# Performance work log

Hardware: AMD Instinct MI355X
Metric: run time of the kernel (lower is better)

Reference implementation:

```python
import jax, jax.numpy as jnp
import numpy as np

RCUT, RCUT_SMTH = 6.0, 0.5
SEL = [32, 64]
SEC = [0, 32, 96]
PAIRS = [(0, 0), (0, 1), (1, 1)]  # (ti, tj) with ti <= tj, matching stacked weight index
NF, NLOC, NALL = 1, 256, 512
NNEI = sum(SEL)
NG = 96


def setup_inputs() -> dict:
    key = jax.random.key(0)
    ks = jax.random.split(key, 10)
    # coords in a 4A cube so most neighbor distances are inside rcut=6
    extended_coord = jax.random.uniform(ks[0], (NF, NALL * 3), dtype=jnp.float32) * 4.0
    nl = jax.random.randint(ks[1], (NF, NLOC, NNEI), 0, NALL - 1)
    # shift indices >= own local index by 1 to avoid self-neighbors (zero distance)
    nlist = nl + (nl >= jnp.arange(NLOC)[None, :, None]).astype(nl.dtype)
    extended_atype = jax.random.randint(ks[2], (NF, NALL), 0, 2)
    mean = jnp.zeros((2, NNEI, 4), jnp.float32)
    stddev = jnp.ones((2, NNEI, 4), jnp.float32)
    def w(k, shape, fan):
        return jax.random.normal(k, shape, jnp.float32) / np.float32(np.sqrt(fan))
    W1 = w(ks[3], (3, 1, 24), 1.0)
    b1 = 0.1 * jax.random.normal(ks[4], (3, 24), jnp.float32)
    W2 = w(ks[5], (3, 24, 48), 24.0)
    b2 = 0.1 * jax.random.normal(ks[6], (3, 48), jnp.float32)
    W3 = w(ks[7], (3, 48, 96), 48.0)
    b3 = 0.1 * jax.random.normal(ks[8], (3, 96), jnp.float32)
    return dict(nlist=nlist, extended_coord=extended_coord, extended_atype=extended_atype,
                mean=mean, stddev=stddev, W1=W1, b1=b1, W2=W2, b2=b2, W3=W3, b3=b3)


def _smooth_weight(r, rmin, rmax):
    uu = (r - rmin) / (rmax - rmin)
    vv = uu * uu * uu * (-6.0 * uu * uu + 15.0 * uu - 10.0) + 1.0
    return jnp.where(r <= rmin, 1.0, jnp.where(r >= rmax, 0.0, vv))


def _env_mat(nlist, coord, atype, mean, stddev):
    nf, nloc, nnei = nlist.shape
    coord = coord.reshape(nf, -1, 3)
    mask = nlist >= 0
    nl = jnp.where(mask, nlist, 0)
    # gather neighbor coords: nf x nloc x nnei x 3
    coord_r = jnp.take_along_axis(coord, nl.reshape(nf, -1, 1), axis=1).reshape(nf, nloc, nnei, 3)
    diff = coord_r - coord[:, :nloc, None, :]
    length = jnp.linalg.norm(diff, axis=-1, keepdims=True)
    length = length + (~mask)[..., None].astype(diff.dtype)  # avoid 0-div on padded entries
    t0 = 1.0 / length
    t1 = diff / (length * length)
    sw = _smooth_weight(length, RCUT_SMTH, RCUT) * mask[..., None].astype(diff.dtype)
    env = jnp.concatenate([t0, t1], axis=-1) * sw  # nf x nloc x nnei x 4
    loc_type = atype[:, :nloc]
    dmatrix = (env - mean[loc_type]) / stddev[loc_type]
    return dmatrix, sw


def _embed(x, W1, b1, W2, b2, W3, b3):
    # EmbeddingNet 1->24->48->96, tanh, resnet doubling residuals
    h1 = jnp.tanh(x @ W1 + b1)
    h2 = jnp.tanh(h1 @ W2 + b2) + jnp.concatenate([h1, h1], axis=-1)
    h3 = jnp.tanh(h2 @ W3 + b3) + jnp.concatenate([h2, h2], axis=-1)
    return h3


def reference(nlist, extended_coord, extended_atype, mean, stddev, W1, b1, W2, b2, W3, b3):
    nf, nloc, nnei = nlist.shape
    dmatrix, sw = _env_mat(nlist, extended_coord, extended_atype, mean, stddev)
    dm = dmatrix.reshape(nf * nloc, nnei, 4)
    result = jnp.zeros((nf * nloc, NG), dm.dtype)
    for p, (ti, tj) in enumerate(PAIRS):
        rr_i = dm[:, SEC[ti]:SEC[ti + 1], 1:]  # nfnl x nt_i x 3
        rr_j = dm[:, SEC[tj]:SEC[tj + 1], 1:]  # nfnl x nt_j x 3
        env_ij = jnp.einsum('ijm,ikm->ijk', rr_i, rr_j)  # nfnl x nt_i x nt_j
        gg = _embed(env_ij[..., None], W1[p], b1[p], W2[p], b2[p], W3[p], b3[p])
        res_ij = jnp.einsum('ijk,ijkm->im', env_ij, gg)
        result = result + res_ij * (1.0 / (SEL[ti] * SEL[tj]))
    return result.reshape(nf, nloc, NG)
```

## Files before the change

### kernel.cpp

```cpp
#include <hip/hip_runtime.h>

#define NLOC 256
#define NNEI 96
#define NG   96
#define H1W  28
#define H2W  52
#define S2LE 2.88539008177793f

typedef __attribute__((ext_vector_type(8))) short short8;
typedef __attribute__((ext_vector_type(4))) float f32x4;
union Frag { uint4 u; short8 s; };

__device__ __forceinline__ float tanh_sc(float s) {
    float e = __builtin_amdgcn_exp2f(s);
    return 1.0f - 2.0f * __builtin_amdgcn_rcpf(e + 1.0f);
}
__device__ __forceinline__ unsigned short f2bf(float f) {
    unsigned int u = __float_as_uint(f);
    u += 0x7FFFu + ((u >> 16) & 1u);
    return (unsigned short)(u >> 16);
}
__device__ __forceinline__ unsigned short f2bf_rhu(float f) {
    return (unsigned short)((__float_as_uint(f) + 0x8000u) >> 16);
}
__device__ __forceinline__ unsigned int pack_bf2(float lo, float hi) {
    unsigned int a = __float_as_uint(lo) + 0x8000u;
    unsigned int b = __float_as_uint(hi) + 0x8000u;
    return __builtin_amdgcn_perm(b, a, 0x07060302);
}

__global__ __launch_bounds__(256) void prep_kernel(
        const float* __restrict__ W1, const float* __restrict__ b1,
        const float* __restrict__ W2, const float* __restrict__ b2,
        const float* __restrict__ W3, const float* __restrict__ b3,
        unsigned short* __restrict__ wf2, unsigned short* __restrict__ wf3,
        unsigned short* __restrict__ wfJ,
        float* __restrict__ w1s, float* __restrict__ b1s,
        float* __restrict__ b2s, float* __restrict__ b3s) {
    int t = blockIdx.x * blockDim.x + threadIdx.x;
    if (t < 2880) {
        int p = t / 960;
        int r = t % 960;
        int tile = r / 64;
        int l = r % 64;
        int nlo = l & 15, g = l >> 4;
        short8 v;
        if (tile < 3) {
            int nt = tile;
            #pragma unroll
            for (int j = 0; j < 8; j++) {
                int k = g * 8 + j;
                float w = (k < 24) ? W2[(p * 24 + k) * 48 + nt * 16 + nlo] * S2LE : 0.0f;
                v[j] = (short)f2bf(w);
            }
            *(short8*)(wf2 + ((p * 3 + nt) * 64 + l) * 8) = v;
        } else {
            int tt = tile - 3;
            int nt = tt >> 1, kc = tt & 1;
            #pragma unroll
            for (int j = 0; j < 8; j++) {
                int kk = (kc == 0) ? (g * 8 + j) : ((j < 4) ? (32 + g * 4 + j) : -1);
                float w = (kk >= 0) ? W3[(p * 48 + kk) * 96 + nt * 16 + nlo] * S2LE : 0.0f;
                v[j] = (short)f2bf(w);
            }
            *(short8*)(wf3 + ((p * 12 + nt * 2 + kc) * 64 + l) * 8) = v;
        }
    } else if (t < 3264) {
        int t2 = t - 2880;
        int f = t2 >> 6, l = t2 & 63;
        int ml = l & 15, g = l >> 4;
        short8 v;
        if (f < 3) {
            int c24 = (f * 16 + ml) % 24;
            #pragma unroll
            for (int j = 0; j < 8; j++)
                v[j] = (short)((g * 8 + j == c24) ? 0x3F80 : 0);
        } else {
            int nt2 = f - 3;
            if (nt2 < 2) {
                int c = nt2 * 16 + ml;
                #pragma unroll
                for (int j = 0; j < 8; j++)
                    v[j] = (short)((g * 8 + j == c) ? 0x3F80 : 0);
            } else {
                #pragma unroll
                for (int j = 0; j < 8; j++)
                    v[j] = (short)((j < 4 && (g * 4 + j) == ml) ? 0x3F80 : 0);
            }
        }
        *(short8*)(wfJ + (f * 64 + l) * 8) = v;
    } else if (t < 3768) {
        int u = t - 3264;
        if (u < 72)       { w1s[u] = W1[u] * S2LE; b1s[u] = b1[u] * S2LE; }
        else if (u < 216) { b2s[u - 72]  = b2[u - 72]  * S2LE; }
        else              { b3s[u - 216] = b3[u - 216] * S2LE; }
    }
}

__launch_bounds__(256, 4)
__global__ void mlp_kernel(const int* __restrict__ nlist, const float* __restrict__ coord,
                           const int* __restrict__ atype,
                           const float* __restrict__ mean, const float* __restrict__ stddev,
                           const float* __restrict__ w1s, const float* __restrict__ b1s,
                           const float* __restrict__ b2s, const float* __restrict__ b3s,
                           const unsigned short* __restrict__ wf2,
                           const unsigned short* __restrict__ wf3,
                           const unsigned short* __restrict__ wfJ,
                           float* __restrict__ out) {
    __shared__ __align__(16) unsigned char smem[40960];
    unsigned short* h1s = (unsigned short*)smem;
    unsigned short* h2s = (unsigned short*)(smem + 14336);
    float* rrl = (float*)(smem + 39808);
    unsigned char* h2b = (unsigned char*)h2s;

    int tid = threadIdx.x;
    int blk = blockIdx.x;
    int i = blk / 20;
    int b = blk - i * 20;

    int p, base_e, offi, offj, count, Aint;
    float scale;
    bool tri;
    if (b < 3)       { p=0; base_e=b*256;      offi=0;  offj=0;  scale=1.0f/1024.0f; count=528;  tri=true;  Aint=65;  }
    else if (b < 11) { p=1; base_e=(b-3)*256;  offi=0;  offj=32; scale=1.0f/2048.0f; count=2048; tri=false; Aint=0;   }
    else             { p=2; base_e=(b-11)*256; offi=32; offj=32; scale=1.0f/4096.0f; count=2080; tri=true;  Aint=129; }

    if (tid < NNEI) {
        int n = tid;
        int idx = nlist[i * NNEI + n];
        bool msk = idx >= 0;
        int safe = msk ? idx : 0;
        float cx = coord[i*3], cy = coord[i*3+1], cz = coord[i*3+2];
        float dx = coord[safe*3]   - cx;
        float dy = coord[safe*3+1] - cy;
        float dz = coord[safe*3+2] - cz;
        float rn = sqrtf(dx*dx + dy*dy + dz*dz) + (msk ? 0.0f : 1.0f);
        float sw;
        if (rn <= 0.5f)      sw = 1.0f;
        else if (rn >= 6.0f) sw = 0.0f;
        else {
            float uu = (rn - 0.5f) * (1.0f / 5.5f);
            sw = uu*uu*uu*(uu*(-6.0f*uu + 15.0f) - 10.0f) + 1.0f;
        }
        if (!msk) sw = 0.0f;
        float ir2 = 1.0f / (rn * rn);
        int ty = atype[i];
        const float* mu = mean   + (ty * NNEI + n) * 4;
        const float* sd = stddev + (ty * NNEI + n) * 4;
        rrl[n*3+0] = (dx * ir2 * sw - mu[1]) / sd[1];
        rrl[n*3+1] = (dy * ir2 * sw - mu[2]) / sd[2];
        rrl[n*3+2] = (dz * ir2 * sw - mu[3]) / sd[3];
    }
    __syncthreads();

    float xs;
    {
        int e = base_e + tid;
        bool valid = e < count;
        int ec = valid ? e : 0;
        int jj, kk;
        float mult = 1.0f;
        if (!tri) { jj = ec >> 6; kk = ec & 63; }
        else {
            float Af = (float)Aint;
            int j = (int)((Af - sqrtf(Af*Af - 8.0f*(float)ec)) * 0.5f);
            int Tj1 = ((j+1)*(Aint-j-1)) >> 1;
            if (ec >= Tj1) j++;
            int Tj = (j*(Aint-j)) >> 1;
            if (ec < Tj) { j--; Tj = (j*(Aint-j)) >> 1; }
            jj = j; kk = j + (ec - Tj);
            mult = (jj == kk) ? 1.0f : 2.0f;
        }
        const float* ri = rrl + (offi + jj) * 3;
        const float* rj = rrl + (offj + kk) * 3;
        float x = ri[0]*rj[0] + ri[1]*rj[1] + ri[2]*rj[2];
        x = valid ? x : 0.0f;
        xs = x * mult;

        const float* w1 = w1s + p * 24;
        const float* c1 = b1s + p * 24;
        float h1v[24];
        #pragma unroll
        for (int u = 0; u < 24; u++)
            h1v[u] = tanh_sc(fmaf(x, w1[u], c1[u]));
        #pragma unroll
        for (int t4 = 0; t4 < 6; t4++) {
            uint2 q = { pack_bf2(h1v[4*t4], h1v[4*t4+1]),
                        pack_bf2(h1v[4*t4+2], h1v[4*t4+3]) };
            *(uint2*)(h1s + tid*H1W + 4*t4) = q;
        }
        uint2 z2 = {0u, 0u};
        *(uint2*)(h1s + tid*H1W + 24) = z2;
        if (tid == 0) *(uint2*)h2s = z2;
    }
    __syncthreads();

    *(float*)(h2b + tid*104 + 96) = xs;
    if (tid < NG) *(float*)(h2b + tid*104 + 100) = 0.0f;

    int l  = tid & 63;
    int w  = tid >> 6;
    int ml = l & 15, g = l >> 4;

    short8 bw2[3], jf2[3];
    float  b2c[3];
    #pragma unroll
    for (int nt = 0; nt < 3; nt++) {
        bw2[nt] = *(const short8*)(wf2 + ((p*3 + nt)*64 + l)*8);
        jf2[nt] = *(const short8*)(wfJ + (nt*64 + l)*8);
        b2c[nt] = b2s[p*48 + nt*16 + ml];
    }
    #pragma unroll
    for (int mi = 0; mi < 4; mi++) {
        int mt = w*4 + mi;
        int arow = mt*16 + ml;
        uint2 lo = *(const uint2*)(h1s + arow*H1W + g*8);
        uint2 hi = *(const uint2*)(h1s + arow*H1W + g*8 + 4);
        Frag fa; fa.u = make_uint4(lo.x, lo.y, hi.x, hi.y);
        #pragma unroll
        for (int nt = 0; nt < 3; nt++) {
            f32x4 bini = {b2c[nt], b2c[nt], b2c[nt], b2c[nt]};
            f32x4 zz   = {0.f, 0.f, 0.f, 0.f};
            f32x4 acc = __builtin_amdgcn_mfma_f32_16x16x32_bf16(fa.s, bw2[nt], bini, 0, 0, 0);
            f32x4 aj  = __builtin_amdgcn_mfma_f32_16x16x32_bf16(fa.s, jf2[nt], zz,   0, 0, 0);
            int col = nt*16 + ml;
            #pragma unroll
            for (int r = 0; r < 4; r++) {
                int orow = mt*16 + g*4 + r;
                float v = tanh_sc(acc[r]) + aj[r];
                h2s[orow*H2W + col] = f2bf_rhu(v);
            }
        }
    }
    __syncthreads();

    short8 a3a[4], a3b[4];
    float  xv[4][4];
    #pragma unroll
    for (int mi = 0; mi < 4; mi++) {
        int mt = w*4 + mi;
        int arow = mt*16 + ml;
        uint2 lo = *(const uint2*)(h2s + arow*H2W + g*8);
        uint2 hi = *(const uint2*)(h2s + arow*H2W + g*8 + 4);
        Frag fa; fa.u = make_uint4(lo.x, lo.y, hi.x, hi.y);
        a3a[mi] = fa.s;
        uint2 t2 = *(const uint2*)(h2s + arow*H2W + 32 + g*4);
        Frag fb; fb.u = make_uint4(t2.x, t2.y, 0u, 0u);
        a3b[mi] = fb.s;
        #pragma unroll
        for (int r = 0; r < 4; r++)
            xv[mi][r] = *(const float*)(h2b + (mt*16 + g*4 + r)*104 + 96);
    }
    short8 jf3[3];
    #pragma unroll
    for (int q = 0; q < 3; q++)
        jf3[q] = *(const short8*)(wfJ + ((3 + q)*64 + l)*8);

    #pragma unroll
    for (int nt2 = 0; nt2 < 3; nt2++) {
        f32x4 zz = {0.f, 0.f, 0.f, 0.f};
        f32x4 aj[4];
        #pragma unroll
        for (int mi = 0; mi < 4; mi++)
            aj[mi] = __builtin_amdgcn_mfma_f32_16x16x32_bf16(
                (nt2 == 2) ? a3b[mi] : a3a[mi], jf3[nt2], zz, 0, 0, 0);
        #pragma unroll
        for (int h = 0; h < 2; h++) {
            int nt = nt2 + 3*h;
            short8 b30 = *(const short8*)(wf3 + ((p*12 + nt*2 + 0)*64 + l)*8);
            short8 b31 = *(const short8*)(wf3 + ((p*12 + nt*2 + 1)*64 + l)*8);
            float b3c = b3s[p*96 + nt*16 + ml];
            float facc = 0.0f;
            #pragma unroll
            for (int mi = 0; mi < 4; mi++) {
                f32x4 bini = {b3c, b3c, b3c, b3c};
                f32x4 acc = __builtin_amdgcn_mfma_f32_16x16x32_bf16(a3a[mi], b30, bini, 0, 0, 0);
                acc = __builtin_amdgcn_mfma_f32_16x16x32_bf16(a3b[mi], b31, acc, 0, 0, 0);
                #pragma unroll
                for (int r = 0; r < 4; r++) {
                    float h3 = tanh_sc(acc[r]) + aj[mi][r];
                    facc += xv[mi][r] * h3;
                }
            }
            facc += __shfl_xor(facc, 16, 64);
            facc += __shfl_xor(facc, 32, 64);
            if (g == 0) atomicAdd((float*)(h2b + (nt*16 + ml)*104 + 100), facc);
        }
    }
    __syncthreads();
    if (tid < NG)
        atomicAdd(&out[i*NG + tid], *(const float*)(h2b + tid*104 + 100) * scale);
}

extern "C" void kernel_launch(void* const* d_in, const int* in_sizes, int n_in,
                              void* d_out, int out_size, void* d_ws, size_t ws_size,
                              hipStream_t stream) {
    const int*   nlist  = (const int*)  d_in[0];
    const float* coord  = (const float*)d_in[1];
    const int*   atype  = (const int*)  d_in[2];
    const float* mean   = (const float*)d_in[3];
    const float* stddev = (const float*)d_in[4];
    const float* W1     = (const float*)d_in[5];
    const float* b1     = (const float*)d_in[6];
    const float* W2     = (const float*)d_in[7];
    const float* b2     = (const float*)d_in[8];
    const float* W3     = (const float*)d_in[9];
    const float* b3     = (const float*)d_in[10];
    float* out = (float*)d_out;

    char* ws = (char*)d_ws;
    unsigned short* wf2 = (unsigned short*)(ws + 0);
    unsigned short* wf3 = (unsigned short*)(ws + 9216);
    unsigned short* wfJ = (unsigned short*)(ws + 46080);
    float* w1s = (float*)(ws + 52224);
    float* b1s = (float*)(ws + 52512);
    float* b2s = (float*)(ws + 52800);
    float* b3s = (float*)(ws + 53376);

    prep_kernel<<<15, 256, 0, stream>>>(W1, b1, W2, b2, W3, b3,
                                        wf2, wf3, wfJ, w1s, b1s, b2s, b3s);
    mlp_kernel<<<NLOC * 20, 256, 0, stream>>>(
        nlist, coord, atype, mean, stddev,
        w1s, b1s, b2s, b3s, wf2, wf3, wfJ, out);
}
```

Measured before the change: 140.5 us.

## Alias h1/h2 shared buffers, store xs as bf16, atomically add directly to global

Shared memory drops from 40 KB to about 27 KB. h2 now overlays the h1 region: h2 values are held in registers as packed bf16 until a barrier, then written. The per-row x multiplier is stored as bf16 in a small separate array. The in-LDS reduction and final barrier are removed, so each wave issues scaled atomicAdds straight to global output. Launch bounds rise to 6 blocks per CU to exploit the smaller footprint, at the cost of register pressure, more global atomics, and bf16 rounding of the x weights.

```diff
diff --git a/kernel.cpp b/kernel.cpp
--- a/kernel.cpp
+++ b/kernel.cpp
@@ -27,6 +27,12 @@
     unsigned int a = __float_as_uint(lo) + 0x8000u;
     unsigned int b = __float_as_uint(hi) + 0x8000u;
     return __builtin_amdgcn_perm(b, a, 0x07060302);
+}
+__device__ __forceinline__ float bfbits_lo(unsigned int u) {
+    return __uint_as_float(u << 16);
+}
+__device__ __forceinline__ float bfbits_hi(unsigned int u) {
+    return __uint_as_float(u & 0xFFFF0000u);
 }
 
 __global__ __launch_bounds__(256) void prep_kernel(
@@ -97,7 +103,7 @@
     }
 }
 
-__launch_bounds__(256, 4)
+__launch_bounds__(256, 6)
 __global__ void mlp_kernel(const int* __restrict__ nlist, const float* __restrict__ coord,
                            const int* __restrict__ atype,
                            const float* __restrict__ mean, const float* __restrict__ stddev,
@@ -107,11 +113,11 @@
                            const unsigned short* __restrict__ wf3,
                            const unsigned short* __restrict__ wfJ,
                            float* __restrict__ out) {
-    __shared__ __align__(16) unsigned char smem[40960];
+    __shared__ __align__(16) unsigned char smem[27136];
     unsigned short* h1s = (unsigned short*)smem;
-    unsigned short* h2s = (unsigned short*)(smem + 14336);
-    float* rrl = (float*)(smem + 39808);
-    unsigned char* h2b = (unsigned char*)h2s;
+    unsigned short* h2s = (unsigned short*)smem;
+    float* rrl = (float*)(smem + 14344);
+    unsigned short* xsb = (unsigned short*)(smem + 26624);
 
     int tid = threadIdx.x;
     int blk = blockIdx.x;
@@ -153,7 +159,6 @@
     }
     __syncthreads();
 
-    float xs;
     {
         int e = base_e + tid;
         bool valid = e < count;
@@ -175,7 +180,7 @@
         const float* rj = rrl + (offj + kk) * 3;
         float x = ri[0]*rj[0] + ri[1]*rj[1] + ri[2]*rj[2];
         x = valid ? x : 0.0f;
-        xs = x * mult;
+        xsb[tid] = f2bf_rhu(x * mult);
 
         const float* w1 = w1s + p * 24;
         const float* c1 = b1s + p * 24;
@@ -191,12 +196,9 @@
         }
         uint2 z2 = {0u, 0u};
         *(uint2*)(h1s + tid*H1W + 24) = z2;
-        if (tid == 0) *(uint2*)h2s = z2;
+        if (tid == 0) *(uint2*)(smem + 14336) = z2;
     }
     __syncthreads();
-
-    *(float*)(h2b + tid*104 + 96) = xs;
-    if (tid < NG) *(float*)(h2b + tid*104 + 100) = 0.0f;
 
     int l  = tid & 63;
     int w  = tid >> 6;
@@ -210,6 +212,7 @@
         jf2[nt] = *(const short8*)(wfJ + (nt*64 + l)*8);
         b2c[nt] = b2s[p*48 + nt*16 + ml];
     }
+    unsigned int h2p[4][3][2];
     #pragma unroll
     for (int mi = 0; mi < 4; mi++) {
         int mt = w*4 + mi;
@@ -223,13 +226,26 @@
             f32x4 zz   = {0.f, 0.f, 0.f, 0.f};
             f32x4 acc = __builtin_amdgcn_mfma_f32_16x16x32_bf16(fa.s, bw2[nt], bini, 0, 0, 0);
             f32x4 aj  = __builtin_amdgcn_mfma_f32_16x16x32_bf16(fa.s, jf2[nt], zz,   0, 0, 0);
+            float v0 = tanh_sc(acc[0]) + aj[0];
+            float v1 = tanh_sc(acc[1]) + aj[1];
+            float v2 = tanh_sc(acc[2]) + aj[2];
+            float v3 = tanh_sc(acc[3]) + aj[3];
+            h2p[mi][nt][0] = pack_bf2(v0, v1);
+            h2p[mi][nt][1] = pack_bf2(v2, v3);
+        }
+    }
+    __syncthreads();
+
+    #pragma unroll
+    for (int mi = 0; mi < 4; mi++) {
+        int orow0 = (w*4 + mi)*16 + g*4;
+        #pragma unroll
+        for (int nt = 0; nt < 3; nt++) {
             int col = nt*16 + ml;
-            #pragma unroll
-            for (int r = 0; r < 4; r++) {
-                int orow = mt*16 + g*4 + r;
-                float v = tanh_sc(acc[r]) + aj[r];
-                h2s[orow*H2W + col] = f2bf_rhu(v);
-            }
+            h2s[(orow0+0)*H2W + col] = (unsigned short)(h2p[mi][nt][0]);
+            h2s[(orow0+1)*H2W + col] = (unsigned short)(h2p[mi][nt][0] >> 16);
+            h2s[(orow0+2)*H2W + col] = (unsigned short)(h2p[mi][nt][1]);
+            h2s[(orow0+3)*H2W + col] = (unsigned short)(h2p[mi][nt][1] >> 16);
         }
     }
     __syncthreads();
@@ -247,15 +263,18 @@
         uint2 t2 = *(const uint2*)(h2s + arow*H2W + 32 + g*4);
         Frag fb; fb.u = make_uint4(t2.x, t2.y, 0u, 0u);
         a3b[mi] = fb.s;
-        #pragma unroll
-        for (int r = 0; r < 4; r++)
-            xv[mi][r] = *(const float*)(h2b + (mt*16 + g*4 + r)*104 + 96);
+        uint2 q = *(const uint2*)(xsb + mt*16 + g*4);
+        xv[mi][0] = bfbits_lo(q.x);
+        xv[mi][1] = bfbits_hi(q.x);
+        xv[mi][2] = bfbits_lo(q.y);
+        xv[mi][3] = bfbits_hi(q.y);
     }
     short8 jf3[3];
     #pragma unroll
     for (int q = 0; q < 3; q++)
         jf3[q] = *(const short8*)(wfJ + ((3 + q)*64 + l)*8);
 
+    float* outrow = out + i*NG;
     #pragma unroll
     for (int nt2 = 0; nt2 < 3; nt2++) {
         f32x4 zz = {0.f, 0.f, 0.f, 0.f};
@@ -284,12 +303,9 @@
             }
             facc += __shfl_xor(facc, 16, 64);
             facc += __shfl_xor(facc, 32, 64);
-            if (g == 0) atomicAdd((float*)(h2b + (nt*16 + ml)*104 + 100), facc);
-        }
-    }
-    __syncthreads();
-    if (tid < NG)
-        atomicAdd(&out[i*NG + tid], *(const float*)(h2b + tid*104 + 100) * scale);
+            if (g == 0) atomicAdd(&outrow[nt*16 + ml], facc * scale);
+        }
+    }
 }
 
 extern "C" void kernel_launch(void* const* d_in, const int* in_sizes, int n_in,
```

Result: slower. 196.0 us (+39.6%).
